# Performance work log

Hardware: AMD Instinct MI355X
Metric: run time of the kernel (lower is better)

## Reference

```python
import jax, jax.numpy as jnp
import numpy as np

CAPACITY_FACTOR = 1.0


def setup_inputs() -> dict:
    key = jax.random.key(0)
    k1, k2, k3 = jax.random.split(key, 3)
    x = jax.random.normal(k1, (4, 2048, 2048), jnp.float32)          # [B, S, d_model]
    wg = jax.random.normal(k2, (2048, 8), jnp.float32) * 0.02        # gate weight [d_model, E]
    we = jax.random.normal(k3, (8, 2048, 8192), jnp.float32) * 0.02  # expert weights [E, d_model, d_ff]
    be = jnp.zeros((8, 8192), jnp.float32)                           # expert bias [E, d_ff]
    return {"x": x, "wg": wg, "we": we, "be": be}


def reference(x, wg, we, be):
    d = x.shape[-1]
    tokens = x.reshape(-1, d)                       # [S, d]  (S = total tokens)
    S = tokens.shape[0]
    E = wg.shape[1]
    C = int(S * CAPACITY_FACTOR) // E               # per-expert capacity

    # ---- top-1 gate (DeepSpeed-style) -> dispatch_mask [S, E, C] ----
    logits = tokens @ wg                            # [S, E]
    gates = jax.nn.softmax(logits, axis=-1)
    idx = jnp.argmax(gates, axis=-1)                # chosen expert per token
    mask1 = jax.nn.one_hot(idx, E, dtype=tokens.dtype)        # [S, E]
    locations = jnp.cumsum(mask1, axis=0) - 1.0               # position within expert queue
    mask1 = mask1 * (locations < C).astype(tokens.dtype)      # drop tokens over capacity
    loc_s = jnp.sum(locations * mask1, axis=1).astype(jnp.int32)  # [S]
    loc_oh = jax.nn.one_hot(loc_s, C, dtype=tokens.dtype)          # [S, C]
    dispatch_mask = mask1[:, :, None] * loc_oh[:, None, :]         # [S, E, C] one-hot

    # ---- dense one-hot dispatch: einsum('sec,sm->ecm') ----
    dispatched = jnp.einsum('sec,sm->ecm', dispatch_mask, tokens)  # [E, C, d]

    # AllToAll with ep_size=1 is identity; reshape (ep_size, num_local_experts, C, d)
    dispatched = dispatched.reshape(1, E, C, d)

    # ---- front experts: per-expert Linear (front half of FFN) ----
    out = jnp.einsum('gecd,edf->gecf', dispatched, we) + be[None, :, None, :]

    return out.reshape(-1, we.shape[-1])            # [E*C, d_ff]
```

## Files before the change

### kernel.cpp

```cpp
#include <hip/hip_runtime.h>
#include <hip/hip_bf16.h>

#define S_TOK 8192
#define DM    2048
#define DFF   8192
#define NE    8
#define CAP   1024

typedef __bf16 bf16_t;
typedef __bf16 bf16x8 __attribute__((ext_vector_type(8)));
typedef float  f32x4  __attribute__((ext_vector_type(4)));

__device__ __forceinline__ void load_lds16(const void* g, void* l) {
    __builtin_amdgcn_global_load_lds((const __attribute__((address_space(1))) void*)g,
                                     (__attribute__((address_space(3))) void*)l,
                                     16, 0, 0);
}

__global__ __launch_bounds__(256) void gate_argmax(const float* __restrict__ x,
                                                   const float* __restrict__ wg,
                                                   int* __restrict__ eidx) {
    int lane = threadIdx.x & 63, wv = threadIdx.x >> 6;
    int s = blockIdx.x * 4 + wv;
    const float* row = x + (size_t)s * DM;
    float acc[8] = {0.f,0.f,0.f,0.f,0.f,0.f,0.f,0.f};
    for (int kb = 0; kb < DM; kb += 256) {
        int k0 = kb + lane * 4;
        float4 xv = *(const float4*)(row + k0);
        const float* wr = wg + (size_t)k0 * NE;
        float xs[4] = {xv.x, xv.y, xv.z, xv.w};
#pragma unroll
        for (int c = 0; c < 4; ++c) {
            float4 w0 = *(const float4*)(wr + c * 8);
            float4 w1 = *(const float4*)(wr + c * 8 + 4);
            acc[0] += xs[c] * w0.x; acc[1] += xs[c] * w0.y;
            acc[2] += xs[c] * w0.z; acc[3] += xs[c] * w0.w;
            acc[4] += xs[c] * w1.x; acc[5] += xs[c] * w1.y;
            acc[6] += xs[c] * w1.z; acc[7] += xs[c] * w1.w;
        }
    }
#pragma unroll
    for (int off = 32; off > 0; off >>= 1)
#pragma unroll
        for (int e = 0; e < 8; ++e) acc[e] += __shfl_xor(acc[e], off, 64);
    if (lane == 0) {
        float best = acc[0]; int bi = 0;
#pragma unroll
        for (int e = 1; e < 8; ++e) if (acc[e] > best) { best = acc[e]; bi = e; }
        eidx[s] = bi;
    }
}

__global__ __launch_bounds__(64) void scatter_slots(const int* __restrict__ eidx,
                                                    int* __restrict__ srcOf) {
    int lane = threadIdx.x;
    unsigned long long below = (lane == 0) ? 0ull : ((1ull << lane) - 1ull);
    for (int i = lane; i < NE * CAP; i += 64) srcOf[i] = -1;

    int cnt[NE] = {0,0,0,0,0,0,0,0};
    int e_cur = eidx[lane];
    for (int it = 0; it < S_TOK / 64; ++it) {
        int e_nxt = (it < S_TOK / 64 - 1) ? eidx[(it + 1) * 64 + lane] : 0;
        int s = it * 64 + lane;
#pragma unroll
        for (int ex = 0; ex < NE; ++ex) {
            unsigned long long m = __ballot(e_cur == ex);
            if (e_cur == ex) {
                int loc = cnt[ex] + __popcll(m & below);
                if (loc < CAP) srcOf[ex * CAP + loc] = s;
            }
            cnt[ex] += __popcll(m);
        }
        e_cur = e_nxt;
    }
}

__global__ __launch_bounds__(256) void pack_rows(const float* __restrict__ x,
                                                 const int* __restrict__ srcOf,
                                                 char* __restrict__ abuf) {
    int slot = blockIdx.x;
    int e = slot >> 10, c = slot & 1023;
    int mt = c >> 8, m = c & 255;
    int src = srcOf[slot];
    int tid = threadIdx.x;
    int kt = tid >> 3, kg = tid & 7;
    bf16x8 v = {};
    if (src >= 0) {
        const float4* p = (const float4*)(x + (size_t)src * DM + kt * 64 + kg * 8);
        float4 a = p[0], b = p[1];
        v = bf16x8{(bf16_t)a.x,(bf16_t)a.y,(bf16_t)a.z,(bf16_t)a.w,
                   (bf16_t)b.x,(bf16_t)b.y,(bf16_t)b.z,(bf16_t)b.w};
    }
    size_t img = ((size_t)((e * 4 + mt) * 32 + kt)) << 15;
    int off = m * 128 + ((kg * 16) ^ ((m & 7) << 4));
    *(bf16x8*)(abuf + img + off) = v;
}

__global__ __launch_bounds__(512, 2) void moe_gemm(const char* __restrict__ abuf,
                                                   const float* __restrict__ we,
                                                   const float* __restrict__ be,
                                                   float* __restrict__ out) {
    __shared__ uint4 smem4[131072 / 16];
    char* smem = (char*)smem4;

    int bid = blockIdx.x;
    int e  = bid & 7;
    int r  = bid >> 3;
    int mt = r & 3;
    int nt = r >> 2;
    int tid = threadIdx.x, lane = tid & 63, wv = tid >> 6;
    int wm = wv >> 2, wn = wv & 3;
    int lr = lane & 15, g = lane >> 4;

    const char* aImg = abuf + (((size_t)((e * 4 + mt) * 32)) << 15);
    const float* bBase = we + (size_t)e * DM * DFF + (size_t)nt * 256 + lane * 4;

    int colx[2];
    colx[0] = (((0 * 4 + g) ^ (lr & 7)) << 4);
    colx[1] = (((1 * 4 + g) ^ (lr & 7)) << 4);
    int aRow = wm * 128 + lr;
    int bRow = wn * 64 + lr;

    int stOff = tid * 16;

    f32x4 acc[8][4] = {};
    float bs[32];

    auto stage_issue = [&](int kt, int buf) {
        const float* bp = bBase + (size_t)(kt * 64 + wv * 8) * DFF;
#pragma unroll
        for (int j = 0; j < 8; ++j) {
            float4 t = *(const float4*)(bp + (size_t)j * DFF);
            bs[j * 4 + 0] = t.x; bs[j * 4 + 1] = t.y;
            bs[j * 4 + 2] = t.z; bs[j * 4 + 3] = t.w;
        }
        const char* src = aImg + ((size_t)kt << 15) + stOff;
        char* dst = smem + buf * 65536 + stOff;
#pragma unroll
        for (int i = 0; i < 4; ++i) load_lds16(src + i * 8192, dst + i * 8192);
    };

    auto stage_writeB = [&](int buf) {
        char* bL = smem + buf * 65536 + 32768;
#pragma unroll
        for (int i = 0; i < 4; ++i) {
            int n = lane * 4 + i;
            bf16x8 w;
#pragma unroll
            for (int j = 0; j < 8; ++j) w[j] = (bf16_t)bs[j * 4 + i];
            *(bf16x8*)(bL + n * 128 + ((wv * 16) ^ ((n & 7) << 4))) = w;
        }
    };

    stage_issue(0, 0);
    stage_writeB(0);
    __syncthreads();

    for (int kt = 0; kt < 32; ++kt) {
        int cur = kt & 1, nxt = cur ^ 1;
        bool notlast = (kt < 31);
        if (notlast) stage_issue(kt + 1, nxt);

        const char* aC = smem + cur * 65536;
        const char* bC = aC + 32768;
#pragma unroll
        for (int mh = 0; mh < 2; ++mh) {
            bf16x8 af[4][2];
#pragma unroll
            for (int mf = 0; mf < 4; ++mf) {
                int rowm = aRow + (mh * 4 + mf) * 16;
                af[mf][0] = *(const bf16x8*)(aC + rowm * 128 + colx[0]);
                af[mf][1] = *(const bf16x8*)(aC + rowm * 128 + colx[1]);
            }
#pragma unroll
            for (int nh = 0; nh < 2; ++nh) {
                bf16x8 bf[2][2];
#pragma unroll
                for (int nf = 0; nf < 2; ++nf) {
                    int rown = bRow + (nh * 2 + nf) * 16;
                    bf[nf][0] = *(const bf16x8*)(bC + rown * 128 + colx[0]);
                    bf[nf][1] = *(const bf16x8*)(bC + rown * 128 + colx[1]);
                }
                __builtin_amdgcn_s_setprio(1);
#pragma unroll
                for (int mf = 0; mf < 4; ++mf)
#pragma unroll
                    for (int nf = 0; nf < 2; ++nf)
#pragma unroll
                        for (int kk = 0; kk < 2; ++kk)
                            acc[mh * 4 + mf][nh * 2 + nf] =
                                __builtin_amdgcn_mfma_f32_16x16x32_bf16(
                                    af[mf][kk], bf[nf][kk],
                                    acc[mh * 4 + mf][nh * 2 + nf], 0, 0, 0);
                __builtin_amdgcn_s_setprio(0);
            }
        }
        if (notlast) stage_writeB(nxt);
        __syncthreads();
    }

    int orow0 = e * CAP + mt * 256 + wm * 128 + g * 4;
    int ocol0 = nt * 256 + wn * 64 + lr;
#pragma unroll
    for (int nf = 0; nf < 4; ++nf) {
        int oc = ocol0 + nf * 16;
        float bias = be[(size_t)e * DFF + oc];
#pragma unroll
        for (int mf = 0; mf < 8; ++mf) {
            int orow = orow0 + mf * 16;
#pragma unroll
            for (int q = 0; q < 4; ++q)
                out[(size_t)(orow + q) * DFF + oc] = acc[mf][nf][q] + bias;
        }
    }
}

extern "C" void kernel_launch(void* const* d_in, const int* in_sizes, int n_in,
                              void* d_out, int out_size, void* d_ws, size_t ws_size,
                              hipStream_t stream) {
    const float* x  = (const float*)d_in[0];
    const float* wg = (const float*)d_in[1];
    const float* we = (const float*)d_in[2];
    const float* be = (const float*)d_in[3];
    float* out = (float*)d_out;

    size_t need = 65536 + (size_t)8 * 4 * 32 * 32768;
    if (ws_size < need) return;

    int* eidx  = (int*)d_ws;
    int* srcOf = eidx + S_TOK;
    char* abuf = (char*)d_ws + 65536;

    gate_argmax<<<S_TOK / 4, 256, 0, stream>>>(x, wg, eidx);
    scatter_slots<<<1, 64, 0, stream>>>(eidx, srcOf);
    pack_rows<<<S_TOK, 256, 0, stream>>>(x, srcOf, abuf);
    moe_gemm<<<NE * 4 * 32, 512, 0, stream>>>(abuf, we, be, out);
}
```

Baseline: 524.2 us.

## Split B staging into two halves interleaved with MFMA, new LDS swizzle

The fp32 expert-weight tile staging is split into two halves of 4 rows each. This halves the register buffer for B, and the second half's global loads and bf16 conversion writes are interleaved between the two M-halves of the MFMA loop. The LDS layout for B changes to an XOR swizzle on both low and high row bits, with 8-byte partial writes per half, to reduce bank conflicts on the narrower stores. A sched_barrier is added to pin the issue order of the prefetch. The aim is lower register pressure and better overlap of global latency with compute, at the risk of more, smaller LDS writes.

```diff
diff --git a/kernel.cpp b/kernel.cpp
--- a/kernel.cpp
+++ b/kernel.cpp
@@ -114,72 +114,82 @@
 
     const char* aImg = abuf + (((size_t)((e * 4 + mt) * 32)) << 15);
     const float* bBase = we + (size_t)e * DM * DFF + (size_t)nt * 256 + lane * 4;
-
-    int colx[2];
-    colx[0] = (((0 * 4 + g) ^ (lr & 7)) << 4);
-    colx[1] = (((1 * 4 + g) ^ (lr & 7)) << 4);
-    int aRow = wm * 128 + lr;
-    int bRow = wn * 64 + lr;
-
     int stOff = tid * 16;
 
     f32x4 acc[8][4] = {};
-    float bs[32];
-
-    auto stage_issue = [&](int kt, int buf) {
-        const float* bp = bBase + (size_t)(kt * 64 + wv * 8) * DFF;
-#pragma unroll
-        for (int j = 0; j < 8; ++j) {
+    float bs[16];
+
+    auto issueB = [&](int kt, int h) {
+        const float* bp = bBase + (size_t)(kt * 64 + wv * 8 + h * 4) * DFF;
+#pragma unroll
+        for (int j = 0; j < 4; ++j) {
             float4 t = *(const float4*)(bp + (size_t)j * DFF);
             bs[j * 4 + 0] = t.x; bs[j * 4 + 1] = t.y;
             bs[j * 4 + 2] = t.z; bs[j * 4 + 3] = t.w;
         }
+    };
+    auto issueA = [&](int kt, int buf) {
         const char* src = aImg + ((size_t)kt << 15) + stOff;
         char* dst = smem + buf * 65536 + stOff;
 #pragma unroll
         for (int i = 0; i < 4; ++i) load_lds16(src + i * 8192, dst + i * 8192);
     };
-
-    auto stage_writeB = [&](int buf) {
+    auto writeB = [&](int buf, int h) {
         char* bL = smem + buf * 65536 + 32768;
 #pragma unroll
         for (int i = 0; i < 4; ++i) {
             int n = lane * 4 + i;
-            bf16x8 w;
-#pragma unroll
-            for (int j = 0; j < 8; ++j) w[j] = (bf16_t)bs[j * 4 + i];
-            *(bf16x8*)(bL + n * 128 + ((wv * 16) ^ ((n & 7) << 4))) = w;
+            ushort w[4];
+#pragma unroll
+            for (int j = 0; j < 4; ++j) {
+                bf16_t b = (bf16_t)bs[j * 4 + i];
+                w[j] = __builtin_bit_cast(unsigned short, b);
+            }
+            uint2 pk = { (unsigned)w[0] | ((unsigned)w[1] << 16),
+                         (unsigned)w[2] | ((unsigned)w[3] << 16) };
+            int slot = (n & 7) ^ ((n >> 3) & 7);
+            *(uint2*)(bL + n * 128 + (((unsigned)(wv ^ slot)) << 4) + h * 8) = pk;
         }
     };
 
-    stage_issue(0, 0);
-    stage_writeB(0);
+    issueA(0, 0);
+    issueB(0, 0); writeB(0, 0);
+    issueB(0, 1); writeB(0, 1);
     __syncthreads();
+
+    int aRow = wm * 128 + lr;
+    int bRow = wn * 64 + lr;
+    int xa = lr & 7;
 
     for (int kt = 0; kt < 32; ++kt) {
         int cur = kt & 1, nxt = cur ^ 1;
         bool notlast = (kt < 31);
-        if (notlast) stage_issue(kt + 1, nxt);
-
         const char* aC = smem + cur * 65536;
         const char* bC = aC + 32768;
+
+        if (notlast) { issueA(kt + 1, nxt); issueB(kt + 1, 0); }
+        __builtin_amdgcn_sched_barrier(0);
+
 #pragma unroll
         for (int mh = 0; mh < 2; ++mh) {
             bf16x8 af[4][2];
 #pragma unroll
             for (int mf = 0; mf < 4; ++mf) {
                 int rowm = aRow + (mh * 4 + mf) * 16;
-                af[mf][0] = *(const bf16x8*)(aC + rowm * 128 + colx[0]);
-                af[mf][1] = *(const bf16x8*)(aC + rowm * 128 + colx[1]);
+#pragma unroll
+                for (int kk = 0; kk < 2; ++kk)
+                    af[mf][kk] = *(const bf16x8*)(aC + rowm * 128 + (((kk * 4 + g) ^ xa) << 4));
             }
 #pragma unroll
             for (int nh = 0; nh < 2; ++nh) {
-                bf16x8 bf[2][2];
+                bf16x8 bfr[2][2];
 #pragma unroll
                 for (int nf = 0; nf < 2; ++nf) {
                     int rown = bRow + (nh * 2 + nf) * 16;
-                    bf[nf][0] = *(const bf16x8*)(bC + rown * 128 + colx[0]);
-                    bf[nf][1] = *(const bf16x8*)(bC + rown * 128 + colx[1]);
+                    int xb = (rown & 7) ^ ((rown >> 3) & 7);
+#pragma unroll
+                    for (int kk = 0; kk < 2; ++kk)
+                        bfr[nf][kk] = *(const bf16x8*)(bC + rown * 128 + (((kk * 4 + g) ^ xb) << 4));
                 }
                 __builtin_amdgcn_s_setprio(1);
 #pragma unroll
@@ -190,12 +200,13 @@
                         for (int kk = 0; kk < 2; ++kk)
                             acc[mh * 4 + mf][nh * 2 + nf] =
                                 __builtin_amdgcn_mfma_f32_16x16x32_bf16(
-                                    af[mf][kk], bf[nf][kk],
+                                    af[mf][kk], bfr[nf][kk],
                                     acc[mh * 4 + mf][nh * 2 + nf], 0, 0, 0);
                 __builtin_amdgcn_s_setprio(0);
             }
-        }
-        if (notlast) stage_writeB(nxt);
+            if (mh == 0 && notlast) { writeB(nxt, 0); issueB(kt + 1, 1); }
+        }
+        if (notlast) writeB(nxt, 1);
         __syncthreads();
     }
 
```

Measured after the change: 500.3 us. 1.05x faster.

## Shrink GEMM tiles to 128x128 with single-buffered LDS and more blocks

Applied to the files above, without the earlier changes.

The MoE expert GEMM changes from 256x256 tiles with 512 threads and double-buffered 128KB LDS to 128x128 tiles with 256 threads and a single 32KB LDS buffer. The grid grows to 4096 blocks and the A pack layout is regrouped to 128-row tiles to match. Global B loads are still prefetched into registers, but LDS writes are now fenced by two barriers per k-step. The aim is higher occupancy and better load balance across CUs. In exchange, each block reuses its operands less, so more global and L2 traffic goes to the fp32 weights, and the extra syncs expose more latency.

```diff
diff --git a/kernel.cpp b/kernel.cpp
--- a/kernel.cpp
+++ b/kernel.cpp
@@ -80,7 +80,7 @@
                                                  char* __restrict__ abuf) {
     int slot = blockIdx.x;
     int e = slot >> 10, c = slot & 1023;
-    int mt = c >> 8, m = c & 255;
+    int mt = c >> 7, m = c & 127;
     int src = srcOf[slot];
     int tid = threadIdx.x;
     int kt = tid >> 3, kg = tid & 7;
@@ -91,126 +91,115 @@
         v = bf16x8{(bf16_t)a.x,(bf16_t)a.y,(bf16_t)a.z,(bf16_t)a.w,
                    (bf16_t)b.x,(bf16_t)b.y,(bf16_t)b.z,(bf16_t)b.w};
     }
-    size_t img = ((size_t)((e * 4 + mt) * 32 + kt)) << 15;
-    int off = m * 128 + ((kg * 16) ^ ((m & 7) << 4));
+    size_t img = (size_t)((e * 8 + mt) * 32 + kt) * 16384;
+    int off = m * 128 + ((kg ^ (m & 7)) << 4);
     *(bf16x8*)(abuf + img + off) = v;
 }
 
-__global__ __launch_bounds__(512, 2) void moe_gemm(const char* __restrict__ abuf,
+__global__ __launch_bounds__(256, 3) void moe_gemm(const char* __restrict__ abuf,
                                                    const float* __restrict__ we,
                                                    const float* __restrict__ be,
                                                    float* __restrict__ out) {
-    __shared__ uint4 smem4[131072 / 16];
+    __shared__ uint4 smem4[32768 / 16];
     char* smem = (char*)smem4;
 
     int bid = blockIdx.x;
     int e  = bid & 7;
     int r  = bid >> 3;
-    int mt = r & 3;
-    int nt = r >> 2;
+    int mt = r & 7;
+    int nt = r >> 3;
     int tid = threadIdx.x, lane = tid & 63, wv = tid >> 6;
-    int wm = wv >> 2, wn = wv & 3;
+    int wm = wv >> 1, wn = wv & 1;
     int lr = lane & 15, g = lane >> 4;
 
-    const char* aImg = abuf + (((size_t)((e * 4 + mt) * 32)) << 15);
-    const float* bBase = we + (size_t)e * DM * DFF + (size_t)nt * 256 + lane * 4;
-
-    int colx[2];
-    colx[0] = (((0 * 4 + g) ^ (lr & 7)) << 4);
-    colx[1] = (((1 * 4 + g) ^ (lr & 7)) << 4);
-    int aRow = wm * 128 + lr;
-    int bRow = wn * 64 + lr;
-
-    int stOff = tid * 16;
-
-    f32x4 acc[8][4] = {};
-    float bs[32];
-
-    auto stage_issue = [&](int kt, int buf) {
-        const float* bp = bBase + (size_t)(kt * 64 + wv * 8) * DFF;
-#pragma unroll
-        for (int j = 0; j < 8; ++j) {
-            float4 t = *(const float4*)(bp + (size_t)j * DFF);
-            bs[j * 4 + 0] = t.x; bs[j * 4 + 1] = t.y;
-            bs[j * 4 + 2] = t.z; bs[j * 4 + 3] = t.w;
-        }
-        const char* src = aImg + ((size_t)kt << 15) + stOff;
-        char* dst = smem + buf * 65536 + stOff;
-#pragma unroll
-        for (int i = 0; i < 4; ++i) load_lds16(src + i * 8192, dst + i * 8192);
+    const char* aI = abuf + (size_t)((e * 8 + mt) * 32) * 16384;
+    int q = tid >> 5;
+    int c = (tid & 31) * 4;
+    const float* bBase = we + (size_t)e * DM * DFF + (size_t)nt * 128 + c;
+
+    f32x4 acc[4][4] = {};
+    float4 bs[8];
+
+    auto issueB = [&](int kt) {
+        const float* bp = bBase + ((size_t)kt * 64 + q * 8) * DFF;
+#pragma unroll
+        for (int j = 0; j < 8; ++j)
+            bs[j] = *(const float4*)(bp + (size_t)j * DFF);
     };
-
-    auto stage_writeB = [&](int buf) {
-        char* bL = smem + buf * 65536 + 32768;
+    auto writeB = [&]() {
 #pragma unroll
         for (int i = 0; i < 4; ++i) {
-            int n = lane * 4 + i;
+            int n = c + i;
             bf16x8 w;
 #pragma unroll
-            for (int j = 0; j < 8; ++j) w[j] = (bf16_t)bs[j * 4 + i];
-            *(bf16x8*)(bL + n * 128 + ((wv * 16) ^ ((n & 7) << 4))) = w;
+            for (int j = 0; j < 8; ++j) {
+                float v = (i == 0) ? bs[j].x : (i == 1) ? bs[j].y
+                        : (i == 2) ? bs[j].z : bs[j].w;
+                w[j] = (bf16_t)v;
+            }
+            *(bf16x8*)(smem + 16384 + n * 128 + ((q ^ (n & 7)) << 4)) = w;
         }
     };
-
-    stage_issue(0, 0);
-    stage_writeB(0);
+    auto stageA = [&](int kt) {
+        const char* src = aI + (size_t)kt * 16384 + tid * 16;
+        char* dst = smem + tid * 16;
+#pragma unroll
+        for (int i = 0; i < 4; ++i) load_lds16(src + i * 4096, dst + i * 4096);
+    };
+
+    issueB(0);
+    stageA(0);
+    writeB();
     __syncthreads();
 
     for (int kt = 0; kt < 32; ++kt) {
-        int cur = kt & 1, nxt = cur ^ 1;
-        bool notlast = (kt < 31);
-        if (notlast) stage_issue(kt + 1, nxt);
-
-        const char* aC = smem + cur * 65536;
-        const char* bC = aC + 32768;
-#pragma unroll
-        for (int mh = 0; mh < 2; ++mh) {
-            bf16x8 af[4][2];
-#pragma unroll
-            for (int mf = 0; mf < 4; ++mf) {
-                int rowm = aRow + (mh * 4 + mf) * 16;
-                af[mf][0] = *(const bf16x8*)(aC + rowm * 128 + colx[0]);
-                af[mf][1] = *(const bf16x8*)(aC + rowm * 128 + colx[1]);
-            }
-#pragma unroll
-            for (int nh = 0; nh < 2; ++nh) {
-                bf16x8 bf[2][2];
-#pragma unroll
-                for (int nf = 0; nf < 2; ++nf) {
-                    int rown = bRow + (nh * 2 + nf) * 16;
-                    bf[nf][0] = *(const bf16x8*)(bC + rown * 128 + colx[0]);
-                    bf[nf][1] = *(const bf16x8*)(bC + rown * 128 + colx[1]);
-                }
-                __builtin_amdgcn_s_setprio(1);
-#pragma unroll
-                for (int mf = 0; mf < 4; ++mf)
-#pragma unroll
-                    for (int nf = 0; nf < 2; ++nf)
-#pragma unroll
-                        for (int kk = 0; kk < 2; ++kk)
-                            acc[mh * 4 + mf][nh * 2 + nf] =
-                                __builtin_amdgcn_mfma_f32_16x16x32_bf16(
-                                    af[mf][kk], bf[nf][kk],
-                                    acc[mh * 4 + mf][nh * 2 + nf], 0, 0, 0);
-                __builtin_amdgcn_s_setprio(0);
-            }
-        }
-        if (notlast) stage_writeB(nxt);
-        __syncthreads();
-    }
-
-    int orow0 = e * CAP + mt * 256 + wm * 128 + g * 4;
-    int ocol0 = nt * 256 + wn * 64 + lr;
+        bool nl = (kt < 31);
+        if (nl) issueB(kt + 1);
+        __builtin_amdgcn_sched_barrier(0);
+
+        bf16x8 af[4][2];
+#pragma unroll
+        for (int mf = 0; mf < 4; ++mf) {
+            int m = wm * 64 + mf * 16 + lr;
+#pragma unroll
+            for (int kk = 0; kk < 2; ++kk)
+                af[mf][kk] = *(const bf16x8*)(smem + m * 128 + (((kk * 4 + g) ^ (m & 7)) << 4));
+        }
+#pragma unroll
+        for (int nf = 0; nf < 4; ++nf) {
+            int n = wn * 64 + nf * 16 + lr;
+            bf16x8 bfr[2];
+#pragma unroll
+            for (int kk = 0; kk < 2; ++kk)
+                bfr[kk] = *(const bf16x8*)(smem + 16384 + n * 128 + (((kk * 4 + g) ^ (n & 7)) << 4));
+#pragma unroll
+            for (int mf = 0; mf < 4; ++mf)
+#pragma unroll
+                for (int kk = 0; kk < 2; ++kk)
+                    acc[mf][nf] = __builtin_amdgcn_mfma_f32_16x16x32_bf16(
+                        af[mf][kk], bfr[kk], acc[mf][nf], 0, 0, 0);
+        }
+
+        if (nl) {
+            __syncthreads();
+            stageA(kt + 1);
+            writeB();
+            __syncthreads();
+        }
+    }
+
+    int orow0 = e * CAP + mt * 128 + wm * 64 + g * 4;
+    int ocol0 = nt * 128 + wn * 64 + lr;
 #pragma unroll
     for (int nf = 0; nf < 4; ++nf) {
         int oc = ocol0 + nf * 16;
         float bias = be[(size_t)e * DFF + oc];
 #pragma unroll
-        for (int mf = 0; mf < 8; ++mf) {
+        for (int mf = 0; mf < 4; ++mf) {
             int orow = orow0 + mf * 16;
 #pragma unroll
-            for (int q = 0; q < 4; ++q)
-                out[(size_t)(orow + q) * DFF + oc] = acc[mf][nf][q] + bias;
+            for (int qq = 0; qq < 4; ++qq)
+                out[(size_t)(orow + qq) * DFF + oc] = acc[mf][nf][qq] + bias;
         }
     }
 }
@@ -224,7 +213,7 @@
     const float* be = (const float*)d_in[3];
     float* out = (float*)d_out;
 
-    size_t need = 65536 + (size_t)8 * 4 * 32 * 32768;
+    size_t need = 65536 + (size_t)32 * 1048576;
     if (ws_size < need) return;
 
     int* eidx  = (int*)d_ws;
@@ -234,5 +223,5 @@
     gate_argmax<<<S_TOK / 4, 256, 0, stream>>>(x, wg, eidx);
     scatter_slots<<<1, 64, 0, stream>>>(eidx, srcOf);
     pack_rows<<<S_TOK, 256, 0, stream>>>(x, srcOf, abuf);
-    moe_gemm<<<NE * 4 * 32, 512, 0, stream>>>(abuf, we, be, out);
-}
+    moe_gemm<<<NE * 8 * 64, 256, 0, stream>>>(abuf, we, be, out);
+}
```

Measured after the change: 576.1 us. 9.9% more time.
